# Kernel optimization log

Hardware: AMD Instinct MI355X
Metric: run time of the kernel (lower is better)

The kernel has to match this reference:

```python
import jax, jax.numpy as jnp
import numpy as np

BS, X_DIM, KEY_DIM, N_KEYS, TOPK = 16384, 4096, 512, 4096, 16


def setup_inputs() -> dict:
    key = jax.random.key(0)
    k_x, k_keys, k_w, k_b = jax.random.split(key, 4)
    bound = 1.0 / np.sqrt(X_DIM)  # torch Linear default init range
    return {
        "x": jax.random.normal(k_x, (BS, X_DIM), dtype=jnp.float32),
        "keys": jax.random.normal(k_keys, (N_KEYS, KEY_DIM), dtype=jnp.float32),
        "W": jax.random.uniform(k_w, (KEY_DIM, X_DIM), dtype=jnp.float32, minval=-bound, maxval=bound),
        "b": jax.random.uniform(k_b, (KEY_DIM,), dtype=jnp.float32, minval=-bound, maxval=bound),
        "topk": TOPK,
    }


def reference(x, keys, W, b, topk):
    # query = projection(x): [bs, key_dim]
    query = jnp.einsum("bx,kx->bk", x, W) + b
    # scores = query @ keys^T: [bs, n_keys]
    scores = jnp.einsum("bd,nd->bn", query, keys)
    real_topk = min(keys.shape[0], topk)
    topk_scores, topk_idx = jax.lax.top_k(scores, real_topk)  # [bs, k]
    bs = scores.shape[0]
    rows = jnp.arange(bs)[:, None]
    # scatter topk scores into a zero tensor, then softmax over the full row
    gates = jnp.zeros_like(scores).at[rows, topk_idx].set(topk_scores)
    gates = jax.nn.softmax(gates, axis=1)
    return (gates, scores)
```

## Files before the change

kernel.cpp:

```cpp
#include <hip/hip_runtime.h>
#include <stdint.h>

#define BS_T   16384
#define XDIM   4096
#define KDIM   512
#define NKEYS  4096
#define KTOP   16

typedef _Float16 half8  __attribute__((ext_vector_type(8)));
typedef float    floatx4 __attribute__((ext_vector_type(4)));

__device__ static inline void gload_lds16(const void* g, void* l) {
  __builtin_amdgcn_global_load_lds(
      (const __attribute__((address_space(1))) uint32_t*)(uintptr_t)g,
      (__attribute__((address_space(3))) uint32_t*)(uint32_t)(uintptr_t)l,
      16, 0, 0);
}

__global__ __launch_bounds__(256) void cvt_f32_f16_v(const float* __restrict__ in,
                                                     _Float16* __restrict__ out, int n8) {
  int stride = gridDim.x * 256;
  for (int i = blockIdx.x * 256 + threadIdx.x; i < n8; i += stride) {
    float4 v0 = ((const float4*)in)[2 * i];
    float4 v1 = ((const float4*)in)[2 * i + 1];
    half8 h = { (_Float16)v0.x, (_Float16)v0.y, (_Float16)v0.z, (_Float16)v0.w,
                (_Float16)v1.x, (_Float16)v1.y, (_Float16)v1.z, (_Float16)v1.w };
    ((half8*)out)[i] = h;
  }
}

__global__ __launch_bounds__(512, 2)
void gemm1_fused(const float* __restrict__ X, const _Float16* __restrict__ Wh,
                 const float* __restrict__ bias, _Float16* __restrict__ Q) {
  __shared__ __align__(16) _Float16 ldsA[2][64 * 64];
  __shared__ __align__(16) _Float16 ldsB[2][512 * 64];

  const int tid  = threadIdx.x;
  const int lane = tid & 63;
  const int wid  = tid >> 6;
  const int rowBase = blockIdx.x * 64;
  const int wc  = wid * 64;
  const int l15 = lane & 15;
  const int q4  = lane >> 4;
  const int sub   = lane >> 3;
  const int gslot = (lane & 7) ^ sub;

  const int arow  = tid >> 3;
  const int aslot = tid & 7;
  const float* aSrc = X + (size_t)(rowBase + arow) * XDIM + aslot * 8;
  char* aDst[2];
  aDst[0] = (char*)&ldsA[0][0] + arow * 128 + ((aslot * 16) ^ ((arow & 7) << 4));
  aDst[1] = (char*)&ldsA[1][0] + arow * 128 + ((aslot * 16) ^ ((arow & 7) << 4));

  floatx4 acc[4][4];
  #pragma unroll
  for (int m = 0; m < 4; ++m)
    #pragma unroll
    for (int n = 0; n < 4; ++n)
      acc[m][n] = (floatx4)0.0f;

  auto stageB = [&](int kt, int buf) {
    #pragma unroll
    for (int i = 0; i < 8; ++i) {
      int g = wid * 8 + i;
      gload_lds16(Wh + (size_t)(g * 8 + sub) * XDIM + kt + gslot * 8,
                  (char*)&ldsB[buf][0] + g * 1024);
    }
  };
  auto writeA = [&](float4 v0, float4 v1, int buf) {
    half8 h = { (_Float16)v0.x, (_Float16)v0.y, (_Float16)v0.z, (_Float16)v0.w,
                (_Float16)v1.x, (_Float16)v1.y, (_Float16)v1.z, (_Float16)v1.w };
    *(half8*)aDst[buf] = h;
  };
  auto compute = [&](int buf) {
    const char* bA = (const char*)&ldsA[buf][0];
    const char* bB = (const char*)&ldsB[buf][0];
    #pragma unroll
    for (int ks = 0; ks < 2; ++ks) {
      const int s = ks * 4 + q4;
      half8 a[4], b[4];
      #pragma unroll
      for (int m = 0; m < 4; ++m) {
        int row = m * 16 + l15;
        a[m] = *(const half8*)(bA + row * 128 + ((s * 16) ^ ((row & 7) << 4)));
      }
      #pragma unroll
      for (int n = 0; n < 4; ++n) {
        int row = wc + n * 16 + l15;
        b[n] = *(const half8*)(bB + row * 128 + ((s * 16) ^ ((row & 7) << 4)));
      }
      #pragma unroll
      for (int m = 0; m < 4; ++m)
        #pragma unroll
        for (int n = 0; n < 4; ++n)
          acc[m][n] = __builtin_amdgcn_mfma_f32_16x16x32_f16(a[m], b[n], acc[m][n], 0, 0, 0);
    }
  };

  {
    float4 v0 = *(const float4*)(aSrc + 0);
    float4 v1 = *(const float4*)(aSrc + 4);
    stageB(0, 0);
    writeA(v0, v1, 0);
  }
  __syncthreads();

  int cur = 0;
  #pragma unroll 2
  for (int t = 0; t < 63; ++t) {
    const int ktn = (t + 1) * 64;
    float4 v0 = *(const float4*)(aSrc + ktn);
    float4 v1 = *(const float4*)(aSrc + ktn + 4);
    stageB(ktn, cur ^ 1);
    compute(cur);
    writeA(v0, v1, cur ^ 1);
    __syncthreads();
    cur ^= 1;
  }
  compute(cur);

  #pragma unroll
  for (int m = 0; m < 4; ++m) {
    #pragma unroll
    for (int n = 0; n < 4; ++n) {
      int col = wc + n * 16 + l15;
      float bv = bias[col];
      #pragma unroll
      for (int r = 0; r < 4; ++r) {
        int row = rowBase + m * 16 + q4 * 4 + r;
        Q[(size_t)row * KDIM + col] = (_Float16)(acc[m][n][r] + bv);
      }
    }
  }
}

template<int BM, int BN, int WAVES, int WGN, int MINW>
__global__ __launch_bounds__(WAVES * 64, MINW)
void gemm16(const _Float16* __restrict__ A, const _Float16* __restrict__ B,
            float* __restrict__ outp, int M, int N, int K, int nCol) {
  __shared__ __align__(16) _Float16 ldsA[BM * 64];
  __shared__ __align__(16) _Float16 ldsB[BN * 64];

  const int tid = threadIdx.x;
  const int cpx = gridDim.x >> 3;
  const int bid = (blockIdx.x & 7) * cpx + (blockIdx.x >> 3);
  const int rowBase = (bid / nCol) * BM;
  const int colBase = (bid % nCol) * BN;
  const int lane = tid & 63;
  const int wid  = tid >> 6;
  const int wr = (wid / WGN) * 64;
  const int wc = (wid % WGN) * 64;
  const int l15 = lane & 15;
  const int q4  = lane >> 4;

  const int sub   = lane >> 3;
  const int gslot = (lane & 7) ^ sub;

  constexpr int GROUPS = (BM + BN) / 8;
  constexpr int GPW    = GROUPS / WAVES;

  floatx4 acc[4][4];
  #pragma unroll
  for (int m = 0; m < 4; ++m)
    #pragma unroll
    for (int n = 0; n < 4; ++n)
      acc[m][n] = (floatx4)0.0f;

  for (int kt = 0; kt < K; kt += 64) {
    #pragma unroll
    for (int i = 0; i < GPW; ++i) {
      int g = wid * GPW + i;
      if (g < BM / 8) {
        const _Float16* src = A + (size_t)(rowBase + g * 8 + sub) * K + kt + gslot * 8;
        gload_lds16(src, (char*)ldsA + g * 1024);
      } else {
        int gb = g - BM / 8;
        const _Float16* src = B + (size_t)(colBase + gb * 8 + sub) * K + kt + gslot * 8;
        gload_lds16(src, (char*)ldsB + gb * 1024);
      }
    }
    __syncthreads();

    #pragma unroll
    for (int ks = 0; ks < 2; ++ks) {
      const int s = ks * 4 + q4;
      half8 a[4], b[4];
      #pragma unroll
      for (int m = 0; m < 4; ++m) {
        int row = wr + m * 16 + l15;
        a[m] = *(const half8*)((const char*)ldsA + row * 128 + ((s * 16) ^ ((row & 7) << 4)));
      }
      #pragma unroll
      for (int n = 0; n < 4; ++n) {
        int row = wc + n * 16 + l15;
        b[n] = *(const half8*)((const char*)ldsB + row * 128 + ((s * 16) ^ ((row & 7) << 4)));
      }
      #pragma unroll
      for (int m = 0; m < 4; ++m)
        #pragma unroll
        for (int n = 0; n < 4; ++n)
          acc[m][n] = __builtin_amdgcn_mfma_f32_16x16x32_f16(a[m], b[n], acc[m][n], 0, 0, 0);
    }
    __syncthreads();
  }

  #pragma unroll
  for (int m = 0; m < 4; ++m) {
    #pragma unroll
    for (int n = 0; n < 4; ++n) {
      int col = colBase + wc + n * 16 + l15;
      #pragma unroll
      for (int r = 0; r < 4; ++r) {
        int row = rowBase + wr + m * 16 + q4 * 4 + r;
        outp[(size_t)row * N + col] = acc[m][n][r];
      }
    }
  }
}

__global__ __launch_bounds__(256) void topk_gates_kernel(const float* __restrict__ scores,
                                                         float* __restrict__ gates) {
  __shared__ uint32_t hist[4096];
  __shared__ uint32_t sA[256];
  __shared__ uint32_t av[16], ai[16];
  __shared__ uint32_t sk[KTOP], si[KTOP];
  __shared__ uint32_t cntA, cntC;
  __shared__ int s_p; __shared__ uint32_t s_above;
  __shared__ float gk[KTOP]; __shared__ float s_gother;

  const int tid  = threadIdx.x;
  const int lane = tid & 63;
  const int w    = tid >> 6;
  const float* srow = scores + (size_t)blockIdx.x * NKEYS;

  uint4 z4 = {0, 0, 0, 0};
  #pragma unroll
  for (int i = 0; i < 4; ++i) ((uint4*)hist)[tid + 256 * i] = z4;
  if (tid == 0) { cntA = 0; cntC = 0; }

  uint32_t key[16];
  const int base = (w << 10) + (lane << 4);
  {
    const float4* p4 = (const float4*)(srow + base);
    #pragma unroll
    for (int i = 0; i < 4; ++i) {
      float4 t = p4[i];
      float tv[4] = { t.x, t.y, t.z, t.w };
      #pragma unroll
      for (int c = 0; c < 4; ++c) {
        uint32_t u = __float_as_uint(tv[c]);
        key[i * 4 + c] = u ^ (uint32_t)(((int32_t)u >> 31) | 0x80000000);
      }
    }
  }
  __syncthreads();

  #pragma unroll
  for (int j = 0; j < 16; ++j) atomicAdd(&hist[key[j] >> 20], 1u);
  __syncthreads();

  uint32_t h[16];
  #pragma unroll
  for (int i = 0; i < 16; ++i) h[i] = hist[tid * 16 + i];
  uint32_t sfx[17]; sfx[16] = 0;
  #pragma unroll
  for (int i = 15; i >= 0; --i) sfx[i] = sfx[i + 1] + h[i];
  sA[tid] = sfx[0];
  __syncthreads();
  uint32_t s = sfx[0];
  #pragma unroll
  for (int off = 1; off < 256; off <<= 1) {
    uint32_t add = (tid + off < 256) ? sA[tid + off] : 0;
    __syncthreads();
    s += add; sA[tid] = s;
    __syncthreads();
  }
  const uint32_t exclHi = s - sfx[0];

  #pragma unroll
  for (int i = 0; i < 16; ++i) {
    uint32_t cg = exclHi + sfx[i + 1];
    if (cg < KTOP && cg + h[i] >= KTOP) { s_p = tid * 16 + i; s_above = cg; }
  }
  __syncthreads();
  const uint32_t p = (uint32_t)s_p;
  const uint32_t above = s_above;
  const uint32_t need = KTOP - above;

  uint32_t* ck = hist;
  uint32_t* ci = hist + 2048;
  #pragma unroll
  for (int j = 0; j < 16; ++j) {
    uint32_t b = key[j] >> 20;
    if (b >= p) {
      uint32_t idx = (uint32_t)(base + j);
      if (b > p) { uint32_t pos = atomicAdd(&cntA, 1u); av[pos] = key[j]; ai[pos] = idx; }
      else       { uint32_t pos = atomicAdd(&cntC, 1u); if (pos < 2048u) { ck[pos] = key[j]; ci[pos] = idx; } }
    }
  }
  __syncthreads();

  const uint32_t nA = cntA;
  if (tid < nA) { sk[tid] = av[tid]; si[tid] = ai[tid]; }

  if (w == 0) {
    const uint32_t nC = min(cntC, 2048u);
    for (uint32_t k = 0; k < need; ++k) {
      uint32_t bk = 0, bi = 0xFFFFFFFFu, bp = 0;
      for (uint32_t c = lane; c < nC; c += 64) {
        uint32_t kk = ck[c], ii = ci[c];
        if (kk > bk || (kk == bk && ii < bi)) { bk = kk; bi = ii; bp = c; }
      }
      #pragma unroll
      for (int off = 32; off >= 1; off >>= 1) {
        uint32_t ok = __shfl_down(bk, off);
        uint32_t oi = __shfl_down(bi, off);
        uint32_t op = __shfl_down(bp, off);
        if (ok > bk || (ok == bk && oi < bi)) { bk = ok; bi = oi; bp = op; }
      }
      bp = __shfl(bp, 0);
      if (lane == 0) { ck[bp] = 0; sk[nA + k] = bk; si[nA + k] = bi; }
    }
  }
  __syncthreads();

  if (tid == 0) {
    float f[KTOP]; float mx = 0.f;
    #pragma unroll
    for (int k = 0; k < KTOP; ++k) {
      uint32_t kk = sk[k];
      float fv = (kk & 0x80000000u) ? __uint_as_float(kk ^ 0x80000000u)
                                    : __uint_as_float(~kk);
      f[k] = fv; mx = fmaxf(mx, fv);
    }
    float eo = __expf(-mx);
    float Z = (float)(NKEYS - KTOP) * eo;
    float e[KTOP];
    #pragma unroll
    for (int k = 0; k < KTOP; ++k) { e[k] = __expf(f[k] - mx); Z += e[k]; }
    float inv = 1.f / Z;
    #pragma unroll
    for (int k = 0; k < KTOP; ++k) gk[k] = e[k] * inv;
    s_gother = eo * inv;
  }
  __syncthreads();

  float go = s_gother;
  float4 g4 = { go, go, go, go };
  float* grow = gates + (size_t)blockIdx.x * NKEYS;
  #pragma unroll
  for (int j = 0; j < 4; ++j) ((float4*)grow)[j * 256 + tid] = g4;
  __syncthreads();
  if (tid < KTOP) grow[si[tid]] = gk[tid];
}

extern "C" void kernel_launch(void* const* d_in, const int* in_sizes, int n_in,
                              void* d_out, int out_size, void* d_ws, size_t ws_size,
                              hipStream_t stream) {
  const float* x    = (const float*)d_in[0];
  const float* keys = (const float*)d_in[1];
  const float* W    = (const float*)d_in[2];
  const float* bias = (const float*)d_in[3];
  (void)in_sizes; (void)n_in; (void)out_size; (void)ws_size;

  float* gates  = (float*)d_out;
  float* scores = (float*)d_out + (size_t)BS_T * NKEYS;

  _Float16* W_h = (_Float16*)d_ws;
  _Float16* k_h = W_h + (size_t)KDIM * XDIM;
  _Float16* q_h = k_h + (size_t)NKEYS * KDIM;

  cvt_f32_f16_v<<<dim3(1024), dim3(256), 0, stream>>>(W, W_h, KDIM * XDIM / 8);
  cvt_f32_f16_v<<<dim3(1024), dim3(256), 0, stream>>>(keys, k_h, NKEYS * KDIM / 8);

  gemm1_fused<<<dim3(BS_T / 64), dim3(512), 0, stream>>>(x, W_h, bias, q_h);

  gemm16<128, 128, 4, 2, 3><<<dim3((BS_T / 128) * (NKEYS / 128)), dim3(256), 0, stream>>>(
      q_h, k_h, scores, BS_T, NKEYS, KDIM, NKEYS / 128);

  topk_gates_kernel<<<dim3(BS_T), dim3(256), 0, stream>>>(scores, gates);
}
```

Baseline: 381.1 us.

## Load A tile directly into registers, bypassing LDS staging in projection GEMM

Removes the LDS buffer for the fp32 input tile and has each wave load its A fragments straight from global memory into registers, converting to fp16 just before the MFMA. Next-iteration fragments are prefetched into a second register set. This is meant to cut LDS writes, reads and conversion traffic. In exchange every wave reads the full A tile redundantly from global/L2, and it needs many more registers for the double-buffered fragments.

Result: slower. 713.6 us (+87.2%).

```diff
diff --git a/kernel.cpp b/kernel.cpp
--- a/kernel.cpp
+++ b/kernel.cpp
@@ -32,7 +32,6 @@
 __global__ __launch_bounds__(512, 2)
 void gemm1_fused(const float* __restrict__ X, const _Float16* __restrict__ Wh,
                  const float* __restrict__ bias, _Float16* __restrict__ Q) {
-  __shared__ __align__(16) _Float16 ldsA[2][64 * 64];
   __shared__ __align__(16) _Float16 ldsB[2][512 * 64];
 
   const int tid  = threadIdx.x;
@@ -45,12 +44,9 @@
   const int sub   = lane >> 3;
   const int gslot = (lane & 7) ^ sub;
 
-  const int arow  = tid >> 3;
-  const int aslot = tid & 7;
-  const float* aSrc = X + (size_t)(rowBase + arow) * XDIM + aslot * 8;
-  char* aDst[2];
-  aDst[0] = (char*)&ldsA[0][0] + arow * 128 + ((aslot * 16) ^ ((arow & 7) << 4));
-  aDst[1] = (char*)&ldsA[1][0] + arow * 128 + ((aslot * 16) ^ ((arow & 7) << 4));
+  const float* aBase = X + (size_t)rowBase * XDIM;
+  const size_t aRowOff[4] = { (size_t)(0 * 16 + l15) * XDIM, (size_t)(1 * 16 + l15) * XDIM,
+                              (size_t)(2 * 16 + l15) * XDIM, (size_t)(3 * 16 + l15) * XDIM };
 
   floatx4 acc[4][4];
   #pragma unroll
@@ -67,57 +63,56 @@
                   (char*)&ldsB[buf][0] + g * 1024);
     }
   };
-  auto writeA = [&](float4 v0, float4 v1, int buf) {
-    half8 h = { (_Float16)v0.x, (_Float16)v0.y, (_Float16)v0.z, (_Float16)v0.w,
-                (_Float16)v1.x, (_Float16)v1.y, (_Float16)v1.z, (_Float16)v1.w };
-    *(half8*)aDst[buf] = h;
+  auto loadA = [&](int kt, float4* f) {
+    #pragma unroll
+    for (int m = 0; m < 4; ++m)
+      #pragma unroll
+      for (int ks = 0; ks < 2; ++ks)
+        #pragma unroll
+        for (int j = 0; j < 2; ++j)
+          f[(m * 2 + ks) * 2 + j] =
+              *(const float4*)(aBase + aRowOff[m] + kt + ks * 32 + q4 * 8 + j * 4);
   };
-  auto compute = [&](int buf) {
-    const char* bA = (const char*)&ldsA[buf][0];
-    const char* bB = (const char*)&ldsB[buf][0];
+
+  float4 fA[16];
+  loadA(0, fA);
+  stageB(0, 0);
+  __syncthreads();
+
+  int cur = 0;
+  #pragma unroll 2
+  for (int t = 0; t < 64; ++t) {
+    float4 fN[16];
+    if (t < 63) {
+      loadA((t + 1) * 64, fN);
+      stageB((t + 1) * 64, cur ^ 1);
+    }
+    const char* bB = (const char*)&ldsB[cur][0];
     #pragma unroll
     for (int ks = 0; ks < 2; ++ks) {
       const int s = ks * 4 + q4;
-      half8 a[4], b[4];
-      #pragma unroll
-      for (int m = 0; m < 4; ++m) {
-        int row = m * 16 + l15;
-        a[m] = *(const half8*)(bA + row * 128 + ((s * 16) ^ ((row & 7) << 4)));
-      }
+      half8 b[4];
       #pragma unroll
       for (int n = 0; n < 4; ++n) {
         int row = wc + n * 16 + l15;
         b[n] = *(const half8*)(bB + row * 128 + ((s * 16) ^ ((row & 7) << 4)));
       }
       #pragma unroll
-      for (int m = 0; m < 4; ++m)
+      for (int m = 0; m < 4; ++m) {
+        float4 v0 = fA[(m * 2 + ks) * 2 + 0];
+        float4 v1 = fA[(m * 2 + ks) * 2 + 1];
+        half8 a = { (_Float16)v0.x, (_Float16)v0.y, (_Float16)v0.z, (_Float16)v0.w,
+                    (_Float16)v1.x, (_Float16)v1.y, (_Float16)v1.z, (_Float16)v1.w };
         #pragma unroll
         for (int n = 0; n < 4; ++n)
-          acc[m][n] = __builtin_amdgcn_mfma_f32_16x16x32_f16(a[m], b[n], acc[m][n], 0, 0, 0);
-    }
-  };
-
-  {
-    float4 v0 = *(const float4*)(aSrc + 0);
-    float4 v1 = *(const float4*)(aSrc + 4);
-    stageB(0, 0);
-    writeA(v0, v1, 0);
-  }
-  __syncthreads();
-
-  int cur = 0;
-  #pragma unroll 2
-  for (int t = 0; t < 63; ++t) {
-    const int ktn = (t + 1) * 64;
-    float4 v0 = *(const float4*)(aSrc + ktn);
-    float4 v1 = *(const float4*)(aSrc + ktn + 4);
-    stageB(ktn, cur ^ 1);
-    compute(cur);
-    writeA(v0, v1, cur ^ 1);
-    __syncthreads();
+          acc[m][n] = __builtin_amdgcn_mfma_f32_16x16x32_f16(a, b[n], acc[m][n], 0, 0, 0);
+      }
+    }
+    __syncthreads();
+    #pragma unroll
+    for (int i = 0; i < 16; ++i) fA[i] = fN[i];
     cur ^= 1;
   }
-  compute(cur);
 
   #pragma unroll
   for (int m = 0; m < 4; ++m) {
```

## Split gemm1 into 64x256 column tiles with 256-thread blocks and XCD-aware block remap

Applied to the files above, without the earlier changes.

The projection GEMM now uses 256-thread blocks that each compute a 64-row by 256-column half of Q, which halves the LDS per block and doubles the grid. Block IDs are permuted so consecutive blocks on the same XCD share the same X rows and both column halves. The aim is better occupancy and load balance. The cost is that X is now read and converted to fp16 twice, once per column half. The loop is also restructured into a single 64-iteration form with the A loads split into two row halves per thread.

Result: no change. 384.7 us (+0.9%).

```diff
diff --git a/kernel.cpp b/kernel.cpp
--- a/kernel.cpp
+++ b/kernel.cpp
@@ -29,16 +29,19 @@
   }
 }
 
-__global__ __launch_bounds__(512, 2)
+__global__ __launch_bounds__(256, 2)
 void gemm1_fused(const float* __restrict__ X, const _Float16* __restrict__ Wh,
                  const float* __restrict__ bias, _Float16* __restrict__ Q) {
   __shared__ __align__(16) _Float16 ldsA[2][64 * 64];
-  __shared__ __align__(16) _Float16 ldsB[2][512 * 64];
+  __shared__ __align__(16) _Float16 ldsB[2][256 * 64];
 
   const int tid  = threadIdx.x;
   const int lane = tid & 63;
   const int wid  = tid >> 6;
-  const int rowBase = blockIdx.x * 64;
+  const int cpx  = gridDim.x >> 3;
+  const int bid  = (blockIdx.x & 7) * cpx + (blockIdx.x >> 3);
+  const int rowBase = (bid >> 1) * 64;
+  const int colBase = (bid & 1) * 256;
   const int wc  = wid * 64;
   const int l15 = lane & 15;
   const int q4  = lane >> 4;
@@ -47,10 +50,14 @@
 
   const int arow  = tid >> 3;
   const int aslot = tid & 7;
-  const float* aSrc = X + (size_t)(rowBase + arow) * XDIM + aslot * 8;
-  char* aDst[2];
-  aDst[0] = (char*)&ldsA[0][0] + arow * 128 + ((aslot * 16) ^ ((arow & 7) << 4));
-  aDst[1] = (char*)&ldsA[1][0] + arow * 128 + ((aslot * 16) ^ ((arow & 7) << 4));
+  const float* aSrc0 = X + (size_t)(rowBase + arow) * XDIM + aslot * 8;
+  const float* aSrc1 = aSrc0 + (size_t)32 * XDIM;
+  const int aoff = arow * 128 + ((aslot * 16) ^ ((arow & 7) << 4));
+  char* const aD0 = (char*)&ldsA[0][0] + aoff;
+  char* const aD1 = (char*)&ldsA[1][0] + aoff;
+  const _Float16* const bSrc = Wh + (size_t)(colBase + wc + sub) * XDIM + gslot * 8;
+  char* const bD0 = (char*)&ldsB[0][0] + wid * 8192;
+  char* const bD1 = (char*)&ldsB[1][0] + wid * 8192;
 
   floatx4 acc[4][4];
   #pragma unroll
@@ -59,22 +66,20 @@
     for (int n = 0; n < 4; ++n)
       acc[m][n] = (floatx4)0.0f;
 
-  auto stageB = [&](int kt, int buf) {
-    #pragma unroll
-    for (int i = 0; i < 8; ++i) {
-      int g = wid * 8 + i;
-      gload_lds16(Wh + (size_t)(g * 8 + sub) * XDIM + kt + gslot * 8,
-                  (char*)&ldsB[buf][0] + g * 1024);
-    }
+  auto stageB = [&](int kt, char* bd) {
+    #pragma unroll
+    for (int i = 0; i < 8; ++i)
+      gload_lds16(bSrc + (size_t)i * 8 * XDIM + kt, bd + i * 1024);
   };
-  auto writeA = [&](float4 v0, float4 v1, int buf) {
-    half8 h = { (_Float16)v0.x, (_Float16)v0.y, (_Float16)v0.z, (_Float16)v0.w,
-                (_Float16)v1.x, (_Float16)v1.y, (_Float16)v1.z, (_Float16)v1.w };
-    *(half8*)aDst[buf] = h;
+  auto writeA = [&](char* ad, float4 v00, float4 v01, float4 v10, float4 v11) {
+    half8 h0 = { (_Float16)v00.x, (_Float16)v00.y, (_Float16)v00.z, (_Float16)v00.w,
+                 (_Float16)v01.x, (_Float16)v01.y, (_Float16)v01.z, (_Float16)v01.w };
+    half8 h1 = { (_Float16)v10.x, (_Float16)v10.y, (_Float16)v10.z, (_Float16)v10.w,
+                 (_Float16)v11.x, (_Float16)v11.y, (_Float16)v11.z, (_Float16)v11.w };
+    *(half8*)ad = h0;
+    *(half8*)(ad + 4096) = h1;
   };
-  auto compute = [&](int buf) {
-    const char* bA = (const char*)&ldsA[buf][0];
-    const char* bB = (const char*)&ldsB[buf][0];
+  auto compute = [&](const char* bA, const char* bB) {
     #pragma unroll
     for (int ks = 0; ks < 2; ++ks) {
       const int s = ks * 4 + q4;
@@ -98,32 +103,42 @@
   };
 
   {
-    float4 v0 = *(const float4*)(aSrc + 0);
-    float4 v1 = *(const float4*)(aSrc + 4);
-    stageB(0, 0);
-    writeA(v0, v1, 0);
-  }
-  __syncthreads();
-
-  int cur = 0;
+    float4 v00 = *(const float4*)(aSrc0);
+    float4 v01 = *(const float4*)(aSrc0 + 4);
+    float4 v10 = *(const float4*)(aSrc1);
+    float4 v11 = *(const float4*)(aSrc1 + 4);
+    stageB(0, bD0);
+    writeA(aD0, v00, v01, v10, v11);
+  }
+  __syncthreads();
+
   #pragma unroll 2
-  for (int t = 0; t < 63; ++t) {
-    const int ktn = (t + 1) * 64;
-    float4 v0 = *(const float4*)(aSrc + ktn);
-    float4 v1 = *(const float4*)(aSrc + ktn + 4);
-    stageB(ktn, cur ^ 1);
-    compute(cur);
-    writeA(v0, v1, cur ^ 1);
-    __syncthreads();
-    cur ^= 1;
-  }
-  compute(cur);
+  for (int t = 0; t < 64; ++t) {
+    const int pc = t & 1;
+    const char* bA = pc ? (const char*)&ldsA[1][0] : (const char*)&ldsA[0][0];
+    const char* bB = pc ? (const char*)&ldsB[1][0] : (const char*)&ldsB[0][0];
+    char* adN = pc ? aD0 : aD1;
+    char* bdN = pc ? bD0 : bD1;
+
+    float4 v00, v01, v10, v11;
+    if (t < 63) {
+      const int ktn = (t + 1) * 64;
+      v00 = *(const float4*)(aSrc0 + ktn);
+      v01 = *(const float4*)(aSrc0 + ktn + 4);
+      v10 = *(const float4*)(aSrc1 + ktn);
+      v11 = *(const float4*)(aSrc1 + ktn + 4);
+      stageB(ktn, bdN);
+    }
+    compute(bA, bB);
+    if (t < 63) writeA(adN, v00, v01, v10, v11);
+    __syncthreads();
+  }
 
   #pragma unroll
   for (int m = 0; m < 4; ++m) {
     #pragma unroll
     for (int n = 0; n < 4; ++n) {
-      int col = wc + n * 16 + l15;
+      int col = colBase + wc + n * 16 + l15;
       float bv = bias[col];
       #pragma unroll
       for (int r = 0; r < 4; ++r) {
@@ -373,7 +388,7 @@
   cvt_f32_f16_v<<<dim3(1024), dim3(256), 0, stream>>>(W, W_h, KDIM * XDIM / 8);
   cvt_f32_f16_v<<<dim3(1024), dim3(256), 0, stream>>>(keys, k_h, NKEYS * KDIM / 8);
 
-  gemm1_fused<<<dim3(BS_T / 64), dim3(512), 0, stream>>>(x, W_h, bias, q_h);
+  gemm1_fused<<<dim3((BS_T / 64) * 2), dim3(256), 0, stream>>>(x, W_h, bias, q_h);
 
   gemm16<128, 128, 4, 2, 3><<<dim3((BS_T / 128) * (NKEYS / 128)), dim3(256), 0, stream>>>(
       q_h, k_h, scores, BS_T, NKEYS, KDIM, NKEYS / 128);
```
